# Performance work log

Measured on AMD Instinct MI355X. Metric: run time of the kernel, lower is better.

## Reference

```python
import jax, jax.numpy as jnp
import numpy as np

PH = PW = 7      # aligned output bins (output_size=(aligned_width, aligned_height)=(7,7))
SR = 2           # fixed bilinear sampling ratio per bin (approximates torchvision adaptive ratio)
NUM_LEVELS = 4


def _sample_offsets(n_bins):
    # offsets (in units of bin size) of SR samples per bin: py + (iy+0.5)/SR
    k = jnp.arange(n_bins * SR, dtype=jnp.float32)
    return (k // SR) + ((k % SR) + 0.5) / SR  # [n_bins*SR]


def _bilinear_gather(feat, ys, xs):
    # feat [C,H,W]; ys [N,I]; xs [N,J] -> [N,C,I,J]  (torchvision bilinear_interpolate semantics)
    C, H, W = feat.shape
    vy = (ys >= -1.0) & (ys <= H)
    vx = (xs >= -1.0) & (xs <= W)
    y = jnp.clip(ys, 0.0, H - 1.0)
    x = jnp.clip(xs, 0.0, W - 1.0)
    y0 = jnp.floor(y)
    x0 = jnp.floor(x)
    ly = y - y0
    lx = x - x0
    y0i = y0.astype(jnp.int32)
    x0i = x0.astype(jnp.int32)
    y1i = jnp.minimum(y0i + 1, H - 1)
    x1i = jnp.minimum(x0i + 1, W - 1)

    def g(yi, xi):
        return feat[:, yi[:, :, None], xi[:, None, :]]  # [C,N,I,J]

    w00 = (1.0 - ly)[:, :, None] * (1.0 - lx)[:, None, :]
    w01 = (1.0 - ly)[:, :, None] * lx[:, None, :]
    w10 = ly[:, :, None] * (1.0 - lx)[:, None, :]
    w11 = ly[:, :, None] * lx[:, None, :]
    val = (w00 * g(y0i, x0i) + w01 * g(y0i, x1i)
           + w10 * g(y1i, x0i) + w11 * g(y1i, x1i))  # [C,N,I,J]
    mask = vy[:, :, None] & vx[:, None, :]            # [N,I,J]
    return jnp.where(mask[None], val, 0.0).transpose(1, 0, 2, 3)


def _roi_align_level(feat, boxes):
    # feat [C,H,W], boxes [N,4] xyxy in this level's coords -> [N,C,PH,PW]
    x1, y1, x2, y2 = boxes[:, 0], boxes[:, 1], boxes[:, 2], boxes[:, 3]
    rw = jnp.maximum(x2 - x1, 1.0)
    rh = jnp.maximum(y2 - y1, 1.0)
    bw = rw / PW
    bh = rh / PH
    ys = y1[:, None] + _sample_offsets(PH)[None, :] * bh[:, None]  # [N, PH*SR]
    xs = x1[:, None] + _sample_offsets(PW)[None, :] * bw[:, None]  # [N, PW*SR]
    v = _bilinear_gather(feat, ys, xs)                             # [N,C,PH*SR,PW*SR]
    N, C = v.shape[0], v.shape[1]
    return v.reshape(N, C, PH, SR, PW, SR).mean(axis=(3, 5))       # avg over samples per bin


def setup_inputs() -> dict:
    key = jax.random.key(0)
    kf0, kf1, kf2, kf3, kxy, klev = jax.random.split(key, 6)
    B, C, H0, N = 2, 256, 160, 512
    feats = {}
    for name, k, hw in (("feat0", kf0, 160), ("feat1", kf1, 80), ("feat2", kf2, 40), ("feat3", kf3, 20)):
        feats[name] = jax.random.normal(k, (B, C, hw, hw), dtype=jnp.float32)
    # boxes xyxy in base (pre-scale) coords, in [0, ~19.5]
    xy = jnp.sort(jax.random.uniform(kxy, (B, N, 2, 2), dtype=jnp.float32) * 19.0, axis=2)
    x1y1 = xy[:, :, 0, :]
    x2y2 = xy[:, :, 1, :] + 0.5  # min box size
    # level ids sorted per batch so torch's group-by-level concat order == roi index order
    levels = jnp.sort(jax.random.randint(klev, (B, N), 0, NUM_LEVELS), axis=1).astype(jnp.float32)
    z = jnp.zeros((B, N, 1), dtype=jnp.float32)
    rois = jnp.concatenate(
        [z, x1y1[..., 0:1], x1y1[..., 1:2], x2y2[..., 0:1], x2y2[..., 1:2], z, levels[..., None]], axis=-1)
    feats["rois"] = rois
    return feats


def reference(feat0, feat1, feat2, feat3, rois):
    feats = [feat0, feat1, feat2, feat3]
    B, _, H0, W0 = feat0.shape
    boxes = rois[..., 1:5]   # [B,N,4]
    levels = rois[..., 6]    # [B,N]
    pooled = 0.0
    for l, feat in enumerate(feats):
        H, W = feat.shape[2], feat.shape[3]
        sw = 8.0 * W / W0
        sh = 8.0 * H / H0
        scale = jnp.array([sw, sh, sw, sh], dtype=boxes.dtype)
        pl = jax.vmap(_roi_align_level)(feat, boxes * scale)        # [B,N,C,PH,PW]
        sel = (levels == l).astype(pl.dtype)[..., None, None, None]
        pooled = pooled + sel * pl
    # F.avg_pool2d(kernel_size=2, stride=1): 7x7 -> 6x6
    p = (pooled[..., :-1, :-1] + pooled[..., 1:, :-1]
         + pooled[..., :-1, 1:] + pooled[..., 1:, 1:]) * 0.25
    B_, N_, C, h, w = p.shape
    return p.reshape(B_ * N_, C * h * w)
```

## Files before the change

### kernel.cpp

```cpp
#include <hip/hip_runtime.h>
#include <hip/hip_bf16.h>
#include <hip/hip_fp16.h>


#define PH 7
#define C_CH 256
#define N_ROI 512
#define H0 160

#define P0 25600
#define P1 6400
#define P2 1600
#define P3 400
#define OFF0 0ull
#define OFF1 (OFF0 + 2ull * C_CH * P0)
#define OFF2 (OFF1 + 2ull * C_CH * P1)
#define OFF3 (OFF2 + 2ull * C_CH * P2)
#define WS_HALFS (OFF3 + 2ull * C_CH * P3)

#define NB0 (400 * 8)
#define NB1 (100 * 8)
#define NB2 (25 * 8)
#define NB3 (7 * 8)
#define NB_ALL (NB0 + NB1 + NB2 + NB3)

__global__ __launch_bounds__(256) void transpose_f16_kernel(
    const float* __restrict__ f0, const float* __restrict__ f1,
    const float* __restrict__ f2, const float* __restrict__ f3,
    __half* __restrict__ ws)
{
    __shared__ float tile[64][65];
    int bid = blockIdx.x;
    const float* in; __half* out; int P;
    if (bid < NB0)                  {              in = f0; out = ws + OFF0; P = P0; }
    else if (bid < NB0 + NB1)       { bid -= NB0;  in = f1; out = ws + OFF1; P = P1; }
    else if (bid < NB0 + NB1 + NB2) { bid -= NB0 + NB1; in = f2; out = ws + OFF2; P = P2; }
    else                            { bid -= NB0 + NB1 + NB2; in = f3; out = ws + OFF3; P = P3; }
    const int tiles_p = (P + 63) >> 6;
    const int tp   = bid % tiles_p;
    const int rest = bid / tiles_p;
    const int c0 = (rest & 3) << 6;
    const int b  = rest >> 2;
    const int p0 = tp << 6;

    const int t  = threadIdx.x;
    const int lx = t & 63;
    const int r0 = t >> 6;

    const float* A = in + ((size_t)b * C_CH + c0) * (size_t)P + p0;
    if (p0 + lx < P) {
        #pragma unroll
        for (int k = 0; k < 16; ++k) {
            const int cc = r0 + k * 4;
            tile[cc][lx] = A[(size_t)cc * P + lx];
        }
    }
    __syncthreads();
    __half* To = out + ((size_t)b * P + p0) * C_CH + c0 + lx;
    #pragma unroll
    for (int k = 0; k < 16; ++k) {
        const int pp = r0 + k * 4;
        if (p0 + pp < P)
            To[(size_t)pp * C_CH] = __float2half(tile[lx][pp]);
    }
}

__global__ __launch_bounds__(256) void roialign_kernel(
    const __half* __restrict__ ws,
    const float* __restrict__ rois, float* __restrict__ out)
{
    const int roi = blockIdx.x;
    const int b   = roi / N_ROI;
    const float* r = rois + (size_t)roi * 7;

    __shared__ int   s_y0[14], s_y1[14], s_x0[14], s_x1[14];
    __shared__ float s_ly[14], s_lx[14], s_vy[14], s_vx[14];
    __shared__ float s_out[C_CH * 37];

    const int lev = (int)r[6];
    int H; const __half* ft;
    if      (lev == 0) { H = 160; ft = ws + OFF0; }
    else if (lev == 1) { H = 80;  ft = ws + OFF1; }
    else if (lev == 2) { H = 40;  ft = ws + OFF2; }
    else               { H = 20;  ft = ws + OFF3; }
    const int W = H;
    const int P = H * W;

    const float scale = (8.0f * (float)H) / (float)H0;
    const float x1 = r[1] * scale, y1 = r[2] * scale;
    const float x2 = r[3] * scale, y2 = r[4] * scale;
    const float bw = fmaxf(x2 - x1, 1.0f) * (1.0f / (float)PH);
    const float bh = fmaxf(y2 - y1, 1.0f) * (1.0f / (float)PH);

    const int t = threadIdx.x;
    if (t < 14) {
        const float off = (float)(t >> 1) + 0.25f + 0.5f * (float)(t & 1);
        const float ys  = y1 + off * bh;
        s_vy[t] = (ys >= -1.0f && ys <= (float)H) ? 1.0f : 0.0f;
        const float y  = fminf(fmaxf(ys, 0.0f), (float)(H - 1));
        const float yf = floorf(y);
        s_ly[t] = y - yf;
        const int y0 = (int)yf;
        s_y0[t] = y0 * (W * C_CH);
        s_y1[t] = min(y0 + 1, H - 1) * (W * C_CH);
    } else if (t < 28) {
        const int k = t - 14;
        const float off = (float)(k >> 1) + 0.25f + 0.5f * (float)(k & 1);
        const float xs  = x1 + off * bw;
        s_vx[k] = (xs >= -1.0f && xs <= (float)W) ? 1.0f : 0.0f;
        const float x  = fminf(fmaxf(xs, 0.0f), (float)(W - 1));
        const float xf = floorf(x);
        s_lx[k] = x - xf;
        const int x0 = (int)xf;
        s_x0[k] = x0 * C_CH;
        s_x1[k] = min(x0 + 1, W - 1) * C_CH;
    }
    __syncthreads();

    const int c = t;
    const __half* __restrict__ cbase = ft + (size_t)b * P * C_CH + c;
    float* __restrict__ sOut = s_out + c * 37;

    float prev[PH];

    for (int i = 0; i < PH; ++i) {
        const int   sy0 = 2 * i, sy1 = 2 * i + 1;
        const float lya = s_ly[sy0], vya = s_vy[sy0];
        const float lyb = s_ly[sy1], vyb = s_vy[sy1];
        const __half* __restrict__ ra0 = cbase + s_y0[sy0];
        const __half* __restrict__ ra1 = cbase + s_y1[sy0];
        const __half* __restrict__ rb0 = cbase + s_y0[sy1];
        const __half* __restrict__ rb1 = cbase + s_y1[sy1];

        float cur[PH];
        #pragma unroll
        for (int j = 0; j < PH; ++j) {
            float acc = 0.0f;
            #pragma unroll
            for (int sj = 0; sj < 2; ++sj) {
                const int   sx  = 2 * j + sj;
                const int   x0  = s_x0[sx], x1i = s_x1[sx];
                const float lx  = s_lx[sx], vx  = s_vx[sx];
                {
                    const float f00 = __half2float(ra0[x0]);
                    const float f01 = __half2float(ra0[x1i]);
                    const float f10 = __half2float(ra1[x0]);
                    const float f11 = __half2float(ra1[x1i]);
                    const float top = f00 + lx * (f01 - f00);
                    const float bot = f10 + lx * (f11 - f10);
                    acc += (vya * vx) * (top + lya * (bot - top));
                }
                {
                    const float f00 = __half2float(rb0[x0]);
                    const float f01 = __half2float(rb0[x1i]);
                    const float f10 = __half2float(rb1[x0]);
                    const float f11 = __half2float(rb1[x1i]);
                    const float top = f00 + lx * (f01 - f00);
                    const float bot = f10 + lx * (f11 - f10);
                    acc += (vyb * vx) * (top + lyb * (bot - top));
                }
            }
            cur[j] = acc * 0.25f;
        }

        if (i > 0) {
            float* __restrict__ o = sOut + (i - 1) * 6;
            #pragma unroll
            for (int j = 0; j < 6; ++j)
                o[j] = 0.25f * (prev[j] + prev[j + 1] + cur[j] + cur[j + 1]);
        }
        #pragma unroll
        for (int j = 0; j < PH; ++j) prev[j] = cur[j];
    }

    __syncthreads();
    float* __restrict__ orow = out + (size_t)roi * (C_CH * 36);
    #pragma unroll
    for (int e = t; e < C_CH * 36; e += 256) {
        const int cc = e / 36;
        const int kk = e - 36 * cc;
        orow[e] = s_out[cc * 37 + kk];
    }
}

__global__ __launch_bounds__(256) void roialign_direct_kernel(
    const float* __restrict__ f0, const float* __restrict__ f1,
    const float* __restrict__ f2, const float* __restrict__ f3,
    const float* __restrict__ rois, float* __restrict__ out)
{
    const int roi = blockIdx.x;
    const int b   = roi / N_ROI;
    const float* r = rois + (size_t)roi * 7;

    __shared__ int   s_y0[14], s_y1[14], s_x0[14], s_x1[14];
    __shared__ float s_ly[14], s_lx[14], s_vy[14], s_vx[14];

    const int lev = (int)r[6];
    int H; const float* f;
    if      (lev == 0) { H = 160; f = f0; }
    else if (lev == 1) { H = 80;  f = f1; }
    else if (lev == 2) { H = 40;  f = f2; }
    else               { H = 20;  f = f3; }
    const int W = H;
    const float scale = (8.0f * (float)H) / (float)H0;
    const float x1 = r[1] * scale, y1 = r[2] * scale;
    const float x2 = r[3] * scale, y2 = r[4] * scale;
    const float bw = fmaxf(x2 - x1, 1.0f) * (1.0f / (float)PH);
    const float bh = fmaxf(y2 - y1, 1.0f) * (1.0f / (float)PH);

    const int t = threadIdx.x;
    if (t < 14) {
        const float off = (float)(t >> 1) + 0.25f + 0.5f * (float)(t & 1);
        const float ys  = y1 + off * bh;
        s_vy[t] = (ys >= -1.0f && ys <= (float)H) ? 1.0f : 0.0f;
        const float y  = fminf(fmaxf(ys, 0.0f), (float)(H - 1));
        const float yf = floorf(y);
        s_ly[t] = y - yf;
        const int y0 = (int)yf;
        s_y0[t] = y0 * W;
        s_y1[t] = min(y0 + 1, H - 1) * W;
    } else if (t < 28) {
        const int k = t - 14;
        const float off = (float)(k >> 1) + 0.25f + 0.5f * (float)(k & 1);
        const float xs  = x1 + off * bw;
        s_vx[k] = (xs >= -1.0f && xs <= (float)W) ? 1.0f : 0.0f;
        const float x  = fminf(fmaxf(xs, 0.0f), (float)(W - 1));
        const float xf = floorf(x);
        s_lx[k] = x - xf;
        const int x0 = (int)xf;
        s_x0[k] = x0;
        s_x1[k] = min(x0 + 1, W - 1);
    }
    __syncthreads();

    const int c = t;
    const float* __restrict__ fc = f + ((size_t)b * C_CH + c) * (size_t)(H * W);
    float* __restrict__ o_base = out + (size_t)roi * (C_CH * 36) + (size_t)c * 36;
    float prev[PH];

    for (int i = 0; i < PH; ++i) {
        const int   sy0 = 2 * i, sy1 = 2 * i + 1;
        const float lya = s_ly[sy0], vya = s_vy[sy0];
        const float lyb = s_ly[sy1], vyb = s_vy[sy1];
        const float* ra0 = fc + s_y0[sy0];
        const float* ra1 = fc + s_y1[sy0];
        const float* rb0 = fc + s_y0[sy1];
        const float* rb1 = fc + s_y1[sy1];
        float cur[PH];
        #pragma unroll
        for (int j = 0; j < PH; ++j) {
            float acc = 0.0f;
            #pragma unroll
            for (int sj = 0; sj < 2; ++sj) {
                const int   sx = 2 * j + sj;
                const int   x0 = s_x0[sx], x1i = s_x1[sx];
                const float lx = s_lx[sx], vx = s_vx[sx];
                {
                    const float f00 = ra0[x0], f01 = ra0[x1i];
                    const float f10 = ra1[x0], f11 = ra1[x1i];
                    const float top = f00 + lx * (f01 - f00);
                    const float bot = f10 + lx * (f11 - f10);
                    acc += (vya * vx) * (top + lya * (bot - top));
                }
                {
                    const float f00 = rb0[x0], f01 = rb0[x1i];
                    const float f10 = rb1[x0], f11 = rb1[x1i];
                    const float top = f00 + lx * (f01 - f00);
                    const float bot = f10 + lx * (f11 - f10);
                    acc += (vyb * vx) * (top + lyb * (bot - top));
                }
            }
            cur[j] = acc * 0.25f;
        }
        if (i > 0) {
            float* o = o_base + (size_t)(i - 1) * 6;
            #pragma unroll
            for (int j = 0; j < 6; ++j)
                o[j] = 0.25f * (prev[j] + prev[j + 1] + cur[j] + cur[j + 1]);
        }
        #pragma unroll
        for (int j = 0; j < PH; ++j) prev[j] = cur[j];
    }
}

extern "C" void kernel_launch(void* const* d_in, const int* in_sizes, int n_in,
                              void* d_out, int out_size, void* d_ws, size_t ws_size,
                              hipStream_t stream) {
    const float* f0   = (const float*)d_in[0];
    const float* f1   = (const float*)d_in[1];
    const float* f2   = (const float*)d_in[2];
    const float* f3   = (const float*)d_in[3];
    const float* rois = (const float*)d_in[4];
    float* out = (float*)d_out;

    const int n_rois = in_sizes[4] / 7;
    const size_t need = WS_HALFS * sizeof(__half);

    if (d_ws != nullptr && ws_size >= need) {
        __half* ws = (__half*)d_ws;
        transpose_f16_kernel<<<NB_ALL, 256, 0, stream>>>(f0, f1, f2, f3, ws);
        roialign_kernel<<<n_rois, 256, 0, stream>>>(ws, rois, out);
    } else {
        roialign_direct_kernel<<<n_rois, 256, 0, stream>>>(f0, f1, f2, f3, rois, out);
    }
}
```

Baseline: 166.0 us.

## Vectorize transpose and gather half2 channel pairs with precomputed bilinear weights

The transpose kernel now reads float4 from the NCHW input and writes packed half2 pairs to the NHWC workspace. The ROI kernel has each thread handle two channels through half2 loads, so one block of 256 threads is split into two halves covering overlapping row ranges. Bilinear weights, including the validity mask and the 1/4 sample average, are precomputed once per ROI in shared memory. The goals are fewer, wider memory transactions and less per-sample arithmetic. The cost is an extra shared-memory table, recomputation of one overlapping row, and possible shared-memory bank conflicts from the stride-36 layout.

```diff
diff --git a/kernel.cpp b/kernel.cpp
--- a/kernel.cpp
+++ b/kernel.cpp
@@ -29,39 +29,45 @@
     const float* __restrict__ f2, const float* __restrict__ f3,
     __half* __restrict__ ws)
 {
-    __shared__ float tile[64][65];
+    __shared__ float tile[64 * 65];
     int bid = blockIdx.x;
-    const float* in; __half* out; int P;
-    if (bid < NB0)                  {              in = f0; out = ws + OFF0; P = P0; }
-    else if (bid < NB0 + NB1)       { bid -= NB0;  in = f1; out = ws + OFF1; P = P1; }
-    else if (bid < NB0 + NB1 + NB2) { bid -= NB0 + NB1; in = f2; out = ws + OFF2; P = P2; }
-    else                            { bid -= NB0 + NB1 + NB2; in = f3; out = ws + OFF3; P = P3; }
+    const float* in; __half* outp; int P;
+    if (bid < NB0)                  {              in = f0; outp = ws + OFF0; P = P0; }
+    else if (bid < NB0 + NB1)       { bid -= NB0;  in = f1; outp = ws + OFF1; P = P1; }
+    else if (bid < NB0 + NB1 + NB2) { bid -= NB0 + NB1; in = f2; outp = ws + OFF2; P = P2; }
+    else                            { bid -= NB0 + NB1 + NB2; in = f3; outp = ws + OFF3; P = P3; }
     const int tiles_p = (P + 63) >> 6;
     const int tp   = bid % tiles_p;
     const int rest = bid / tiles_p;
     const int c0 = (rest & 3) << 6;
     const int b  = rest >> 2;
     const int p0 = tp << 6;
-
-    const int t  = threadIdx.x;
-    const int lx = t & 63;
-    const int r0 = t >> 6;
-
-    const float* A = in + ((size_t)b * C_CH + c0) * (size_t)P + p0;
-    if (p0 + lx < P) {
-        #pragma unroll
-        for (int k = 0; k < 16; ++k) {
-            const int cc = r0 + k * 4;
-            tile[cc][lx] = A[(size_t)cc * P + lx];
-        }
-    }
-    __syncthreads();
-    __half* To = out + ((size_t)b * P + p0) * C_CH + c0 + lx;
+    const int pmax = P - p0;
+
+    const int t = threadIdx.x;
+    const int pc  = (t & 15) << 2;
+    const int cc0 = t >> 4;
+    const float* A = in + ((size_t)b * C_CH + c0 + cc0) * (size_t)P + p0 + pc;
+    if (pc < pmax) {
+        #pragma unroll
+        for (int k = 0; k < 4; ++k) {
+            const float4 v = *(const float4*)(A + (size_t)(16 * k) * P);
+            float* dst = tile + (cc0 + 16 * k) * 65 + pc;
+            dst[0] = v.x; dst[1] = v.y; dst[2] = v.z; dst[3] = v.w;
+        }
+    }
+    __syncthreads();
+    const int c2  = t & 31;
+    const int pr0 = t >> 5;
+    __half2* O = (__half2*)outp + ((size_t)b * P + p0) * (C_CH / 2) + (c0 >> 1) + c2;
     #pragma unroll
-    for (int k = 0; k < 16; ++k) {
-        const int pp = r0 + k * 4;
-        if (p0 + pp < P)
-            To[(size_t)pp * C_CH] = __float2half(tile[lx][pp]);
+    for (int k = 0; k < 8; ++k) {
+        const int pp = pr0 + 8 * k;
+        if (pp < pmax) {
+            const float fx = tile[(2 * c2)     * 65 + pp];
+            const float fy = tile[(2 * c2 + 1) * 65 + pp];
+            O[(size_t)pp * (C_CH / 2)] = __floats2half2_rn(fx, fy);
+        }
     }
 }
 
@@ -73,9 +79,10 @@
     const int b   = roi / N_ROI;
     const float* r = rois + (size_t)roi * 7;
 
-    __shared__ int   s_y0[14], s_y1[14], s_x0[14], s_x1[14];
-    __shared__ float s_ly[14], s_lx[14], s_vy[14], s_vx[14];
-    __shared__ float s_out[C_CH * 37];
+    __shared__ int    s_y0[14], s_y1[14], s_x0[14], s_x1[14];
+    __shared__ float  s_ly[14], s_lx[14], s_vy[14], s_vx[14];
+    __shared__ float4 s_w[14][14];
+    __shared__ float  s_out[C_CH * 36];
 
     const int lev = (int)r[6];
     int H; const __half* ft;
@@ -101,8 +108,8 @@
         const float yf = floorf(y);
         s_ly[t] = y - yf;
         const int y0 = (int)yf;
-        s_y0[t] = y0 * (W * C_CH);
-        s_y1[t] = min(y0 + 1, H - 1) * (W * C_CH);
+        s_y0[t] = y0 * (W * (C_CH / 2));
+        s_y1[t] = min(y0 + 1, H - 1) * (W * (C_CH / 2));
     } else if (t < 28) {
         const int k = t - 14;
         const float off = (float)(k >> 1) + 0.25f + 0.5f * (float)(k & 1);
@@ -112,75 +119,75 @@
         const float xf = floorf(x);
         s_lx[k] = x - xf;
         const int x0 = (int)xf;
-        s_x0[k] = x0 * C_CH;
-        s_x1[k] = min(x0 + 1, W - 1) * C_CH;
-    }
-    __syncthreads();
-
-    const int c = t;
-    const __half* __restrict__ cbase = ft + (size_t)b * P * C_CH + c;
-    float* __restrict__ sOut = s_out + c * 37;
-
-    float prev[PH];
-
-    for (int i = 0; i < PH; ++i) {
-        const int   sy0 = 2 * i, sy1 = 2 * i + 1;
-        const float lya = s_ly[sy0], vya = s_vy[sy0];
-        const float lyb = s_ly[sy1], vyb = s_vy[sy1];
-        const __half* __restrict__ ra0 = cbase + s_y0[sy0];
-        const __half* __restrict__ ra1 = cbase + s_y1[sy0];
-        const __half* __restrict__ rb0 = cbase + s_y0[sy1];
-        const __half* __restrict__ rb1 = cbase + s_y1[sy1];
-
-        float cur[PH];
-        #pragma unroll
-        for (int j = 0; j < PH; ++j) {
-            float acc = 0.0f;
+        s_x0[k] = x0 * (C_CH / 2);
+        s_x1[k] = min(x0 + 1, W - 1) * (C_CH / 2);
+    }
+    __syncthreads();
+
+    if (t < 196) {
+        const int sy = t / 14, sx = t - 14 * sy;
+        const float ly = s_ly[sy], lx = s_lx[sx];
+        const float v  = 0.25f * s_vy[sy] * s_vx[sx];
+        const float hy = v * ly;
+        const float my = v - hy;
+        s_w[sy][sx] = make_float4(my - my * lx, my * lx, hy - hy * lx, hy * lx);
+    }
+    __syncthreads();
+
+    const int g  = t >> 7;
+    const int c2 = t & 127;
+    const __half2* __restrict__ cbase =
+        (const __half2*)ft + (size_t)b * P * (C_CH / 2) + c2;
+
+    const int i0 = g ? 3 : 0;
+    const int i1 = g ? 7 : 4;
+    float prevx[7], prevy[7];
+
+    for (int i = i0; i < i1; ++i) {
+        float curx[7], cury[7];
+        #pragma unroll
+        for (int j = 0; j < 7; ++j) { curx[j] = 0.0f; cury[j] = 0.0f; }
+
+        #pragma unroll
+        for (int syk = 0; syk < 2; ++syk) {
+            const int sy = 2 * i + syk;
+            const __half2* __restrict__ q0 = cbase + s_y0[sy];
+            const __half2* __restrict__ q1 = cbase + s_y1[sy];
             #pragma unroll
-            for (int sj = 0; sj < 2; ++sj) {
-                const int   sx  = 2 * j + sj;
-                const int   x0  = s_x0[sx], x1i = s_x1[sx];
-                const float lx  = s_lx[sx], vx  = s_vx[sx];
-                {
-                    const float f00 = __half2float(ra0[x0]);
-                    const float f01 = __half2float(ra0[x1i]);
-                    const float f10 = __half2float(ra1[x0]);
-                    const float f11 = __half2float(ra1[x1i]);
-                    const float top = f00 + lx * (f01 - f00);
-                    const float bot = f10 + lx * (f11 - f10);
-                    acc += (vya * vx) * (top + lya * (bot - top));
-                }
-                {
-                    const float f00 = __half2float(rb0[x0]);
-                    const float f01 = __half2float(rb0[x1i]);
-                    const float f10 = __half2float(rb1[x0]);
-                    const float f11 = __half2float(rb1[x1i]);
-                    const float top = f00 + lx * (f01 - f00);
-                    const float bot = f10 + lx * (f11 - f10);
-                    acc += (vyb * vx) * (top + lyb * (bot - top));
+            for (int j = 0; j < 7; ++j) {
+                #pragma unroll
+                for (int sxk = 0; sxk < 2; ++sxk) {
+                    const int sx = 2 * j + sxk;
+                    const float4 w = s_w[sy][sx];
+                    const int xa = s_x0[sx], xb = s_x1[sx];
+                    const __half2 h00 = q0[xa], h01 = q0[xb];
+                    const __half2 h10 = q1[xa], h11 = q1[xb];
+                    curx[j] += w.x * __low2float(h00)  + w.y * __low2float(h01)
+                             + w.z * __low2float(h10)  + w.w * __low2float(h11);
+                    cury[j] += w.x * __high2float(h00) + w.y * __high2float(h01)
+                             + w.z * __high2float(h10) + w.w * __high2float(h11);
                 }
             }
-            cur[j] = acc * 0.25f;
-        }
-
-        if (i > 0) {
-            float* __restrict__ o = sOut + (i - 1) * 6;
+        }
+
+        if (i > i0) {
+            float* __restrict__ o0 = s_out + (2 * c2)     * 36 + (i - 1) * 6;
+            float* __restrict__ o1 = s_out + (2 * c2 + 1) * 36 + (i - 1) * 6;
             #pragma unroll
-            for (int j = 0; j < 6; ++j)
-                o[j] = 0.25f * (prev[j] + prev[j + 1] + cur[j] + cur[j + 1]);
-        }
-        #pragma unroll
-        for (int j = 0; j < PH; ++j) prev[j] = cur[j];
+            for (int j = 0; j < 6; ++j) {
+                o0[j] = 0.25f * (prevx[j] + prevx[j + 1] + curx[j] + curx[j + 1]);
+                o1[j] = 0.25f * (prevy[j] + prevy[j + 1] + cury[j] + cury[j + 1]);
+            }
+        }
+        #pragma unroll
+        for (int j = 0; j < 7; ++j) { prevx[j] = curx[j]; prevy[j] = cury[j]; }
     }
 
     __syncthreads();
     float* __restrict__ orow = out + (size_t)roi * (C_CH * 36);
     #pragma unroll
-    for (int e = t; e < C_CH * 36; e += 256) {
-        const int cc = e / 36;
-        const int kk = e - 36 * cc;
-        orow[e] = s_out[cc * 37 + kk];
-    }
+    for (int e = t; e < C_CH * 36; e += 256)
+        orow[e] = s_out[e];
 }
 
 __global__ __launch_bounds__(256) void roialign_direct_kernel(
```

After: 146.7 us. 1.13x faster.
